# Kernel tuning notes

Hardware: AMD Instinct MI355X
Metric: run time of the kernel (lower is better)

## Reference

```python
import jax, jax.numpy as jnp
import numpy as np

N = 50000          # nodes
E = 800000         # edges (before self loops)
H = 4              # attention heads
C = 64             # per-head channels
D_IN = 256
NEG_ATT = 0.2      # GATConv attention LeakyReLU slope
NEG_ACT = 0.01     # nn.LeakyReLU default slope
EPS = 1e-5
MLP_DIMS = [64, 32, 16, 2]


def _gat_layer(x, src, dst, W, a_src, a_dst, b, concat):
    """PyG GATConv: gather -> segment-softmax over dst -> scatter-add."""
    n = x.shape[0]
    h = (x @ W).reshape(n, H, C)                       # [N,H,C]
    s = (h * a_src).sum(-1)                            # [N,H]
    d = (h * a_dst).sum(-1)                            # [N,H]
    e = jax.nn.leaky_relu(s[src] + d[dst], NEG_ATT)    # [E',H]
    m = jax.ops.segment_max(e, dst, num_segments=n)    # per-dst max (self loops -> no empty segs)
    w = jnp.exp(e - m[dst])
    den = jax.ops.segment_sum(w, dst, num_segments=n)
    alpha = w / den[dst]                               # [E',H]
    out = jax.ops.segment_sum(alpha[:, :, None] * h[src], dst, num_segments=n)  # [N,H,C]
    out = out.reshape(n, H * C) if concat else out.mean(axis=1)
    return out + b


def _graph_norm(x, w, b, a):
    mu = x.mean(axis=0, keepdims=True)
    y = x - a * mu
    var = (y * y).mean(axis=0, keepdims=True)
    return w * y * jax.lax.rsqrt(var + EPS) + b


def setup_inputs() -> dict:
    key = jax.random.key(0)
    ks = jax.random.split(key, 40)
    d = {
        'x': jax.random.normal(ks[0], (N, D_IN), dtype=jnp.float32),
        'edge_index': jax.random.randint(ks[1], (2, E), 0, N, dtype=jnp.int64),
    }
    dims_in = [D_IN, H * C, H * C]
    norm_dims = [H * C, H * C, C]
    k = 2
    for i in range(3):
        fan = dims_in[i]
        d[f'W{i}'] = jax.random.normal(ks[k], (fan, H * C), dtype=jnp.float32) / np.sqrt(fan); k += 1
        d[f'as{i}'] = jax.random.normal(ks[k], (H, C), dtype=jnp.float32) / np.sqrt(C); k += 1
        d[f'ad{i}'] = jax.random.normal(ks[k], (H, C), dtype=jnp.float32) / np.sqrt(C); k += 1
        d[f'b{i}'] = jnp.zeros((norm_dims[i],), dtype=jnp.float32)
        d[f'gw{i}'] = jnp.ones((norm_dims[i],), dtype=jnp.float32)
        d[f'gb{i}'] = jnp.zeros((norm_dims[i],), dtype=jnp.float32)
        d[f'ga{i}'] = jnp.ones((norm_dims[i],), dtype=jnp.float32)
    for j in range(3):
        fi, fo = MLP_DIMS[j], MLP_DIMS[j + 1]
        d[f'mW{j}'] = jax.random.normal(ks[k], (fi, fo), dtype=jnp.float32) / np.sqrt(fi); k += 1
        d[f'mb{j}'] = jnp.zeros((fo,), dtype=jnp.float32)
    return d


def reference(x, edge_index,
              W0, as0, ad0, b0, gw0, gb0, ga0,
              W1, as1, ad1, b1, gw1, gb1, ga1,
              W2, as2, ad2, b2, gw2, gb2, ga2,
              mW0, mb0, mW1, mb1, mW2, mb2):
    n = x.shape[0]
    loop = jnp.arange(n, dtype=edge_index.dtype)
    src = jnp.concatenate([edge_index[0], loop])   # add self loops (PyG default)
    dst = jnp.concatenate([edge_index[1], loop])

    h = _gat_layer(x, src, dst, W0, as0, ad0, b0, concat=True)
    h = jax.nn.leaky_relu(_graph_norm(h, gw0, gb0, ga0), NEG_ACT)
    h = _gat_layer(h, src, dst, W1, as1, ad1, b1, concat=True)
    h = jax.nn.leaky_relu(_graph_norm(h, gw1, gb1, ga1), NEG_ACT)
    h = _gat_layer(h, src, dst, W2, as2, ad2, b2, concat=False)
    h = jax.nn.leaky_relu(_graph_norm(h, gw2, gb2, ga2), NEG_ACT)

    h = jax.nn.relu(h @ mW0 + mb0)
    h = jax.nn.relu(h @ mW1 + mb1)
    return h @ mW2 + mb2
```

## Files before the change

### kernel.cpp

```cpp
#include <hip/hip_runtime.h>

#define NN 50000
#define EE 800000
#define ET 850000
#define HH 4
#define CC 64
#define FDIM 256

#define SCAN_BLK 512
#define SCAN_NB ((NN + SCAN_BLK - 1) / SCAN_BLK)

typedef unsigned short ushort;
typedef __bf16 bf16x8 __attribute__((ext_vector_type(8)));
typedef float floatx4 __attribute__((ext_vector_type(4)));
typedef ushort ushort8v __attribute__((ext_vector_type(8)));
struct ushort4s { ushort x, y, z, w; };

__device__ __forceinline__ ushort f2bf(float f) {
  union { float f; unsigned u; } v; v.f = f;
  unsigned r = v.u + 0x7fffu + ((v.u >> 16) & 1u);
  return (ushort)(r >> 16);
}
__device__ __forceinline__ float bf2f(ushort u) {
  return __uint_as_float(((unsigned)u) << 16);
}

__device__ __forceinline__ int get_edge(const void* p, int is64, long long idx) {
  if (is64) return (int)((const long long*)p)[idx];
  return ((const int*)p)[idx];
}

__global__ void detect_kernel(const unsigned int* p, int* flag) {
  __shared__ unsigned red[256];
  int t = threadIdx.x;
  unsigned o = 0;
  for (int i = 0; i < 4; i++) o |= p[(t * 4 + i) * 2 + 1];
  red[t] = o;
  __syncthreads();
  for (int s = 128; s > 0; s >>= 1) {
    if (t < s) red[t] |= red[t + s];
    __syncthreads();
  }
  if (t == 0) *flag = (red[0] == 0) ? 1 : 0;
}

__global__ void degree_kernel(const void* eidx, const int* flag, int* deg) {
  int k = blockIdx.x * blockDim.x + threadIdx.x;
  if (k >= ET) return;
  int is64 = *flag;
  int dst = (k < EE) ? get_edge(eidx, is64, (long long)EE + k) : (k - EE);
  atomicAdd(&deg[dst], 1);
}

__global__ __launch_bounds__(SCAN_BLK) void scan1_kernel(const int* __restrict__ deg,
                                                         int* __restrict__ rowptr,
                                                         int* __restrict__ bsum) {
  __shared__ int sm[SCAN_BLK];
  int t = threadIdx.x;
  int i = blockIdx.x * SCAN_BLK + t;
  int v = (i < NN) ? deg[i] : 0;
  sm[t] = v;
  __syncthreads();
#pragma unroll
  for (int o = 1; o < SCAN_BLK; o <<= 1) {
    int u = (t >= o) ? sm[t - o] : 0;
    __syncthreads();
    sm[t] += u;
    __syncthreads();
  }
  if (i < NN) rowptr[i] = sm[t] - v;
  if (t == SCAN_BLK - 1) bsum[blockIdx.x] = sm[t];
}

__global__ __launch_bounds__(128) void scan2_kernel(const int* __restrict__ bsum,
                                                    int* __restrict__ boff,
                                                    int* __restrict__ rowptr) {
  __shared__ int sm[128];
  int t = threadIdx.x;
  int v = (t < SCAN_NB) ? bsum[t] : 0;
  sm[t] = v;
  __syncthreads();
#pragma unroll
  for (int o = 1; o < 128; o <<= 1) {
    int u = (t >= o) ? sm[t - o] : 0;
    __syncthreads();
    sm[t] += u;
    __syncthreads();
  }
  if (t < SCAN_NB) boff[t] = sm[t] - v;
  if (t == 0) rowptr[NN] = ET;
}

__global__ __launch_bounds__(SCAN_BLK) void scan3_kernel(int* __restrict__ rowptr,
                                                         int* __restrict__ cursor,
                                                         const int* __restrict__ boff) {
  int i = blockIdx.x * SCAN_BLK + threadIdx.x;
  if (i >= NN) return;
  int v = rowptr[i] + boff[blockIdx.x];
  rowptr[i] = v;
  cursor[i] = v;
}

__global__ void fill_kernel(const void* eidx, const int* flag, int* cursor, int* csr_src) {
  int k = blockIdx.x * blockDim.x + threadIdx.x;
  if (k >= ET) return;
  int is64 = *flag;
  int src, dst;
  if (k < EE) {
    src = get_edge(eidx, is64, k);
    dst = get_edge(eidx, is64, (long long)EE + k);
  } else {
    src = dst = k - EE;
  }
  int pos = atomicAdd(&cursor[dst], 1);
  csr_src[pos] = src;
}

__global__ void conv_w_kernel(const float* __restrict__ W0, const float* __restrict__ W1,
                              const float* __restrict__ W2,
                              ushort* __restrict__ T0, ushort* __restrict__ T1,
                              ushort* __restrict__ T2) {
  const float* W = (blockIdx.y == 0) ? W0 : (blockIdx.y == 1) ? W1 : W2;
  ushort* Wt = (blockIdx.y == 0) ? T0 : (blockIdx.y == 1) ? T1 : T2;
  int idx = blockIdx.x * 256 + threadIdx.x;
  int k = idx >> 8, n = idx & 255;
  Wt[n * 256 + k] = f2bf(W[idx]);
}

template <int MODE>
__global__ __launch_bounds__(256) void gemm_bf16(const void* __restrict__ Ap,
                                                 const ushort* __restrict__ Bt,
                                                 ushort* __restrict__ C,
                                                 const float* __restrict__ as_,
                                                 const float* __restrict__ ad_,
                                                 float* __restrict__ s_arr,
                                                 float* __restrict__ d_arr,
                                                 const float* __restrict__ colsum,
                                                 const float* __restrict__ colsumsq,
                                                 const float* __restrict__ ga,
                                                 const float* __restrict__ gw,
                                                 const float* __restrict__ gb) {
  __shared__ ushort As[4 * 512];
  __shared__ ushort Bs[8 * 512];
  __shared__ float scs[FDIM], shs[FDIM];
  int tid = threadIdx.x, w = tid >> 6, l = tid & 63;
  int brow0 = blockIdx.x * 64, bcol0 = blockIdx.y * 128;
  int lm = l & 15, lk = (l >> 4) * 8;
  int arA = min(brow0 + w * 16 + lm, NN - 1);
  size_t arowA = (size_t)arA * 256 + lk;
  const ushort* bg0 = Bt + (size_t)(bcol0 + (2 * w) * 16 + lm) * 256 + lk;
  const ushort* bg1 = Bt + (size_t)(bcol0 + (2 * w + 1) * 16 + lm) * 256 + lk;

  if constexpr (MODE == 1) {
    const float invn = 1.0f / (float)NN;
    float mu = colsum[tid] * invn;
    float ex2 = colsumsq[tid] * invn;
    float a = ga[tid];
    float var = fmaxf(ex2 - (2.f * a - a * a) * mu * mu, 0.f);
    float s = gw[tid] * rsqrtf(var + 1e-5f);
    scs[tid] = s;
    shs[tid] = gb[tid] - s * a * mu;
    __syncthreads();
  }

  floatx4 acc[2][4];
#pragma unroll
  for (int i = 0; i < 2; i++)
#pragma unroll
    for (int j = 0; j < 4; j++) acc[i][j] = floatx4{0.f, 0.f, 0.f, 0.f};

  int wm = (w >> 1) * 2, wn = (w & 1) * 4;

  for (int k0 = 0; k0 < 256; k0 += 32) {
    ushort8v a0;
    if constexpr (MODE == 0) {
      const float* p0 = (const float*)Ap + arowA + k0;
      float4 u0 = *(const float4*)p0, v0 = *(const float4*)(p0 + 4);
      a0 = ushort8v{f2bf(u0.x), f2bf(u0.y), f2bf(u0.z), f2bf(u0.w),
                    f2bf(v0.x), f2bf(v0.y), f2bf(v0.z), f2bf(v0.w)};
    } else {
      ushort8v r0 = *(const ushort8v*)((const ushort*)Ap + arowA + k0);
      int kb = k0 + lk;
#pragma unroll
      for (int j = 0; j < 8; j++) {
        float sc = scs[kb + j], sh = shs[kb + j];
        float y0 = fmaf(sc, bf2f(r0[j]), sh);
        y0 = fmaxf(y0, 0.01f * y0);
        a0[j] = f2bf(y0);
      }
    }
    ushort8v b0 = *(const ushort8v*)(bg0 + k0);
    ushort8v b1 = *(const ushort8v*)(bg1 + k0);
    *(ushort8v*)&As[w * 512 + l * 8] = a0;
    *(ushort8v*)&Bs[(2 * w) * 512 + l * 8] = b0;
    *(ushort8v*)&Bs[(2 * w + 1) * 512 + l * 8] = b1;
    __syncthreads();
    bf16x8 af[2], bfr[4];
#pragma unroll
    for (int i = 0; i < 2; i++) af[i] = *(const bf16x8*)&As[(wm + i) * 512 + l * 8];
#pragma unroll
    for (int j = 0; j < 4; j++) bfr[j] = *(const bf16x8*)&Bs[(wn + j) * 512 + l * 8];
#pragma unroll
    for (int i = 0; i < 2; i++)
#pragma unroll
      for (int j = 0; j < 4; j++)
        acc[i][j] = __builtin_amdgcn_mfma_f32_16x16x32_bf16(af[i], bfr[j], acc[i][j], 0, 0, 0);
    __syncthreads();
  }

  int quad = l >> 4;
#pragma unroll
  for (int i = 0; i < 2; i++) {
    int r0 = brow0 + (wm + i) * 16 + quad * 4;
#pragma unroll
    for (int j = 0; j < 4; j++) {
      int col = bcol0 + (wn + j) * 16 + lm;
#pragma unroll
      for (int r = 0; r < 4; r++) {
        int row = r0 + r;
        if (row < NN) C[(size_t)row * 256 + col] = f2bf(acc[i][j][r]);
      }
    }
  }
  float asv[4], adv[4];
#pragma unroll
  for (int j = 0; j < 4; j++) {
    int col = bcol0 + (wn + j) * 16 + lm;
    asv[j] = as_[col];
    adv[j] = ad_[col];
  }
  int head = (bcol0 >> 6) + (w & 1);
#pragma unroll
  for (int i = 0; i < 2; i++) {
#pragma unroll
    for (int r = 0; r < 4; r++) {
      float sp = acc[i][0][r] * asv[0] + acc[i][1][r] * asv[1] +
                 acc[i][2][r] * asv[2] + acc[i][3][r] * asv[3];
      float dp = acc[i][0][r] * adv[0] + acc[i][1][r] * adv[1] +
                 acc[i][2][r] * adv[2] + acc[i][3][r] * adv[3];
      sp += __shfl_xor(sp, 1); dp += __shfl_xor(dp, 1);
      sp += __shfl_xor(sp, 2); dp += __shfl_xor(dp, 2);
      sp += __shfl_xor(sp, 4); dp += __shfl_xor(dp, 4);
      sp += __shfl_xor(sp, 8); dp += __shfl_xor(dp, 8);
      if (lm == 0) {
        int row = brow0 + (wm + i) * 16 + quad * 4 + r;
        if (row < NN) {
          s_arr[row * HH + head] = sp;
          d_arr[row * HH + head] = dp;
        }
      }
    }
  }
}

template <bool CONCAT>
__global__ __launch_bounds__(256) void agg_kernel(const ushort* __restrict__ hb,
                                                  const float* __restrict__ s_arr,
                                                  const float* __restrict__ d_arr,
                                                  const int* __restrict__ rowptr,
                                                  const int* __restrict__ csr_src,
                                                  const float* __restrict__ bias,
                                                  void* __restrict__ outp) {
  int w = __builtin_amdgcn_readfirstlane(threadIdx.x >> 6);
  int l = threadIdx.x & 63;
  int head = l >> 4;
  int n = blockIdx.x * 4 + w;
  int beg = rowptr[n], end = rowptr[n + 1];
  float dh = d_arr[n * HH + head];
  float a0 = 0.f, a1 = 0.f, a2 = 0.f, a3 = 0.f, den = 0.f;

  int i = beg;
  for (; i + 8 <= end; i += 8) {
    int s0 = csr_src[i], s1 = csr_src[i + 1], s2 = csr_src[i + 2], s3 = csr_src[i + 3];
    int s4 = csr_src[i + 4], s5 = csr_src[i + 5], s6 = csr_src[i + 6], s7 = csr_src[i + 7];
    float e0 = s_arr[s0 * HH + head] + dh;
    float e1 = s_arr[s1 * HH + head] + dh;
    float e2 = s_arr[s2 * HH + head] + dh;
    float e3 = s_arr[s3 * HH + head] + dh;
    float e4 = s_arr[s4 * HH + head] + dh;
    float e5 = s_arr[s5 * HH + head] + dh;
    float e6 = s_arr[s6 * HH + head] + dh;
    float e7 = s_arr[s7 * HH + head] + dh;
    ushort4s h0 = *(const ushort4s*)(hb + (unsigned)(s0 * FDIM + l * 4));
    ushort4s h1 = *(const ushort4s*)(hb + (unsigned)(s1 * FDIM + l * 4));
    ushort4s h2 = *(const ushort4s*)(hb + (unsigned)(s2 * FDIM + l * 4));
    ushort4s h3 = *(const ushort4s*)(hb + (unsigned)(s3 * FDIM + l * 4));
    ushort4s h4 = *(const ushort4s*)(hb + (unsigned)(s4 * FDIM + l * 4));
    ushort4s h5 = *(const ushort4s*)(hb + (unsigned)(s5 * FDIM + l * 4));
    ushort4s h6 = *(const ushort4s*)(hb + (unsigned)(s6 * FDIM + l * 4));
    ushort4s h7 = *(const ushort4s*)(hb + (unsigned)(s7 * FDIM + l * 4));
    e0 = (e0 > 0.f) ? e0 : 0.2f * e0;  float w0 = __expf(e0);
    e1 = (e1 > 0.f) ? e1 : 0.2f * e1;  float w1 = __expf(e1);
    e2 = (e2 > 0.f) ? e2 : 0.2f * e2;  float w2 = __expf(e2);
    e3 = (e3 > 0.f) ? e3 : 0.2f * e3;  float w3 = __expf(e3);
    e4 = (e4 > 0.f) ? e4 : 0.2f * e4;  float w4 = __expf(e4);
    e5 = (e5 > 0.f) ? e5 : 0.2f * e5;  float w5 = __expf(e5);
    e6 = (e6 > 0.f) ? e6 : 0.2f * e6;  float w6 = __expf(e6);
    e7 = (e7 > 0.f) ? e7 : 0.2f * e7;  float w7 = __expf(e7);
    den += ((w0 + w1) + (w2 + w3)) + ((w4 + w5) + (w6 + w7));
    a0 = fmaf(w0, bf2f(h0.x), a0); a1 = fmaf(w0, bf2f(h0.y), a1);
    a2 = fmaf(w0, bf2f(h0.z), a2); a3 = fmaf(w0, bf2f(h0.w), a3);
    a0 = fmaf(w1, bf2f(h1.x), a0); a1 = fmaf(w1, bf2f(h1.y), a1);
    a2 = fmaf(w1, bf2f(h1.z), a2); a3 = fmaf(w1, bf2f(h1.w), a3);
    a0 = fmaf(w2, bf2f(h2.x), a0); a1 = fmaf(w2, bf2f(h2.y), a1);
    a2 = fmaf(w2, bf2f(h2.z), a2); a3 = fmaf(w2, bf2f(h2.w), a3);
    a0 = fmaf(w3, bf2f(h3.x), a0); a1 = fmaf(w3, bf2f(h3.y), a1);
    a2 = fmaf(w3, bf2f(h3.z), a2); a3 = fmaf(w3, bf2f(h3.w), a3);
    a0 = fmaf(w4, bf2f(h4.x), a0); a1 = fmaf(w4, bf2f(h4.y), a1);
    a2 = fmaf(w4, bf2f(h4.z), a2); a3 = fmaf(w4, bf2f(h4.w), a3);
    a0 = fmaf(w5, bf2f(h5.x), a0); a1 = fmaf(w5, bf2f(h5.y), a1);
    a2 = fmaf(w5, bf2f(h5.z), a2); a3 = fmaf(w5, bf2f(h5.w), a3);
    a0 = fmaf(w6, bf2f(h6.x), a0); a1 = fmaf(w6, bf2f(h6.y), a1);
    a2 = fmaf(w6, bf2f(h6.z), a2); a3 = fmaf(w6, bf2f(h6.w), a3);
    a0 = fmaf(w7, bf2f(h7.x), a0); a1 = fmaf(w7, bf2f(h7.y), a1);
    a2 = fmaf(w7, bf2f(h7.z), a2); a3 = fmaf(w7, bf2f(h7.w), a3);
  }
  for (; i + 4 <= end; i += 4) {
    int s0 = csr_src[i], s1 = csr_src[i + 1], s2 = csr_src[i + 2], s3 = csr_src[i + 3];
    float e0 = s_arr[s0 * HH + head] + dh;
    float e1 = s_arr[s1 * HH + head] + dh;
    float e2 = s_arr[s2 * HH + head] + dh;
    float e3 = s_arr[s3 * HH + head] + dh;
    ushort4s h0 = *(const ushort4s*)(hb + (unsigned)(s0 * FDIM + l * 4));
    ushort4s h1 = *(const ushort4s*)(hb + (unsigned)(s1 * FDIM + l * 4));
    ushort4s h2 = *(const ushort4s*)(hb + (unsigned)(s2 * FDIM + l * 4));
    ushort4s h3 = *(const ushort4s*)(hb + (unsigned)(s3 * FDIM + l * 4));
    e0 = (e0 > 0.f) ? e0 : 0.2f * e0;  float w0 = __expf(e0);
    e1 = (e1 > 0.f) ? e1 : 0.2f * e1;  float w1 = __expf(e1);
    e2 = (e2 > 0.f) ? e2 : 0.2f * e2;  float w2 = __expf(e2);
    e3 = (e3 > 0.f) ? e3 : 0.2f * e3;  float w3 = __expf(e3);
    den += (w0 + w1) + (w2 + w3);
    a0 = fmaf(w0, bf2f(h0.x), a0); a1 = fmaf(w0, bf2f(h0.y), a1);
    a2 = fmaf(w0, bf2f(h0.z), a2); a3 = fmaf(w0, bf2f(h0.w), a3);
    a0 = fmaf(w1, bf2f(h1.x), a0); a1 = fmaf(w1, bf2f(h1.y), a1);
    a2 = fmaf(w1, bf2f(h1.z), a2); a3 = fmaf(w1, bf2f(h1.w), a3);
    a0 = fmaf(w2, bf2f(h2.x), a0); a1 = fmaf(w2, bf2f(h2.y), a1);
    a2 = fmaf(w2, bf2f(h2.z), a2); a3 = fmaf(w2, bf2f(h2.w), a3);
    a0 = fmaf(w3, bf2f(h3.x), a0); a1 = fmaf(w3, bf2f(h3.y), a1);
    a2 = fmaf(w3, bf2f(h3.z), a2); a3 = fmaf(w3, bf2f(h3.w), a3);
  }
  for (; i < end; i++) {
    int s0 = csr_src[i];
    float e0 = s_arr[s0 * HH + head] + dh;
    ushort4s h0 = *(const ushort4s*)(hb + (unsigned)(s0 * FDIM + l * 4));
    e0 = (e0 > 0.f) ? e0 : 0.2f * e0;
    float w0 = __expf(e0);
    den += w0;
    a0 = fmaf(w0, bf2f(h0.x), a0); a1 = fmaf(w0, bf2f(h0.y), a1);
    a2 = fmaf(w0, bf2f(h0.z), a2); a3 = fmaf(w0, bf2f(h0.w), a3);
  }
  float inv = 1.0f / den;
  float r0 = a0 * inv, r1 = a1 * inv, r2 = a2 * inv, r3 = a3 * inv;

  if (CONCAT) {
    float4 bv = ((const float4*)bias)[l];
    ushort4s o;
    o.x = f2bf(r0 + bv.x); o.y = f2bf(r1 + bv.y);
    o.z = f2bf(r2 + bv.z); o.w = f2bf(r3 + bv.w);
    ((ushort4s*)outp)[(unsigned)(n * 64 + l)] = o;
  } else {
    r0 += __shfl_xor(r0, 16); r1 += __shfl_xor(r1, 16);
    r2 += __shfl_xor(r2, 16); r3 += __shfl_xor(r3, 16);
    r0 += __shfl_xor(r0, 32); r1 += __shfl_xor(r1, 32);
    r2 += __shfl_xor(r2, 32); r3 += __shfl_xor(r3, 32);
    if (l < 16) {
      float4 bv = ((const float4*)bias)[l];
      float4 o;
      o.x = 0.25f * r0 + bv.x; o.y = 0.25f * r1 + bv.y;
      o.z = 0.25f * r2 + bv.z; o.w = 0.25f * r3 + bv.w;
      ((float4*)outp)[(unsigned)(n * 16 + l)] = o;
    }
  }
}

__global__ __launch_bounds__(256) void norm_reduce_bf(const ushort* __restrict__ xin,
                                                      float* colsum, float* colsumsq) {
  __shared__ float4 sm1[256], sm2[256];
  int t = threadIdx.x;
  int c4 = (t & 63) * 4;
  int rl = t >> 6;
  int r0 = blockIdx.x * 128;
  int r1 = min(NN, r0 + 128);
  float s0 = 0.f, s1 = 0.f, s2 = 0.f, s3 = 0.f;
  float q0 = 0.f, q1 = 0.f, q2 = 0.f, q3 = 0.f;
  for (int r = r0 + rl; r < r1; r += 4) {
    ushort4s v = *(const ushort4s*)(xin + (size_t)r * FDIM + c4);
    float f0 = bf2f(v.x), f1 = bf2f(v.y), f2 = bf2f(v.z), f3 = bf2f(v.w);
    s0 += f0; q0 += f0 * f0;
    s1 += f1; q1 += f1 * f1;
    s2 += f2; q2 += f2 * f2;
    s3 += f3; q3 += f3 * f3;
  }
  sm1[t] = float4{s0, s1, s2, s3};
  sm2[t] = float4{q0, q1, q2, q3};
  __syncthreads();
  if (t < 64) {
    float4 a = sm1[t], b = sm1[t + 64], c = sm1[t + 128], d = sm1[t + 192];
    atomicAdd(&colsum[c4 + 0], a.x + b.x + c.x + d.x);
    atomicAdd(&colsum[c4 + 1], a.y + b.y + c.y + d.y);
    atomicAdd(&colsum[c4 + 2], a.z + b.z + c.z + d.z);
    atomicAdd(&colsum[c4 + 3], a.w + b.w + c.w + d.w);
    float4 e = sm2[t], f = sm2[t + 64], g = sm2[t + 128], h = sm2[t + 192];
    atomicAdd(&colsumsq[c4 + 0], e.x + f.x + g.x + h.x);
    atomicAdd(&colsumsq[c4 + 1], e.y + f.y + g.y + h.y);
    atomicAdd(&colsumsq[c4 + 2], e.z + f.z + g.z + h.z);
    atomicAdd(&colsumsq[c4 + 3], e.w + f.w + g.w + h.w);
  }
}

__global__ __launch_bounds__(256) void norm_reduce_f32(const float* __restrict__ xin,
                                                       float* colsum, float* colsumsq) {
  int f = threadIdx.x & (CC - 1);
  int rl = threadIdx.x / CC;
  int r0 = blockIdx.x * 128;
  int r1 = min(NN, r0 + 128);
  float s1 = 0.f, s2 = 0.f;
  for (int r = r0 + rl; r < r1; r += 4) {
    float v = xin[(size_t)r * CC + f];
    s1 += v; s2 += v * v;
  }
  atomicAdd(&colsum[f], s1);
  atomicAdd(&colsumsq[f], s2);
}

__global__ __launch_bounds__(256) void mlp_kernel(const float* __restrict__ xin,
                                                  const float* __restrict__ colsum,
                                                  const float* __restrict__ colsumsq,
                                                  const float* __restrict__ ga,
                                                  const float* __restrict__ gw,
                                                  const float* __restrict__ gb,
                                                  const float* mW0, const float* mb0,
                                                  const float* mW1, const float* mb1,
                                                  const float* mW2, const float* mb2,
                                                  float* __restrict__ out) {
  __shared__ float W0s[64 * 32];
  __shared__ float W1s[32 * 16];
  __shared__ float W2s[16 * 2];
  __shared__ float b0s[32], b1s[16], b2s[2];
  __shared__ float sc[CC], sh[CC];
  int t = threadIdx.x;
  for (int i = t; i < 2048; i += 256) W0s[i] = mW0[i];
  for (int i = t; i < 512; i += 256) W1s[i] = mW1[i];
  if (t < 32) { W2s[t] = mW2[t]; b0s[t] = mb0[t]; }
  if (t < 16) b1s[t] = mb1[t];
  if (t < 2) b2s[t] = mb2[t];
  if (t < CC) {
    const float invn = 1.0f / (float)NN;
    float mu = colsum[t] * invn;
    float ex2 = colsumsq[t] * invn;
    float a = ga[t];
    float var = fmaxf(ex2 - (2.f * a - a * a) * mu * mu, 0.f);
    float s = gw[t] * rsqrtf(var + 1e-5f);
    sc[t] = s; sh[t] = gb[t] - s * a * mu;
  }
  __syncthreads();
  int node = blockIdx.x * 256 + t;
  if (node >= NN) return;
  float in[64];
  const float* xr = xin + (size_t)node * 64;
#pragma unroll
  for (int k = 0; k < 64; k++) {
    float y = sc[k] * xr[k] + sh[k];
    in[k] = (y > 0.f) ? y : 0.01f * y;
  }
  float h1[32];
#pragma unroll
  for (int j = 0; j < 32; j++) h1[j] = b0s[j];
#pragma unroll
  for (int k = 0; k < 64; k++) {
    float v = in[k];
#pragma unroll
    for (int j = 0; j < 32; j++) h1[j] += v * W0s[k * 32 + j];
  }
#pragma unroll
  for (int j = 0; j < 32; j++) h1[j] = fmaxf(h1[j], 0.f);
  float h2[16];
#pragma unroll
  for (int j = 0; j < 16; j++) h2[j] = b1s[j];
#pragma unroll
  for (int k = 0; k < 32; k++) {
    float v = h1[k];
#pragma unroll
    for (int j = 0; j < 16; j++) h2[j] += v * W1s[k * 16 + j];
  }
#pragma unroll
  for (int j = 0; j < 16; j++) h2[j] = fmaxf(h2[j], 0.f);
  float o0 = b2s[0], o1 = b2s[1];
#pragma unroll
  for (int k = 0; k < 16; k++) {
    o0 += h2[k] * W2s[k * 2 + 0];
    o1 += h2[k] * W2s[k * 2 + 1];
  }
  out[(size_t)node * 2 + 0] = o0;
  out[(size_t)node * 2 + 1] = o1;
}

extern "C" void kernel_launch(void* const* d_in, const int* in_sizes, int n_in,
                              void* d_out, int out_size, void* d_ws, size_t ws_size,
                              hipStream_t stream) {
  const float* x = (const float*)d_in[0];
  const void* ei = d_in[1];
  const float* W[3]   = {(const float*)d_in[2],  (const float*)d_in[9],  (const float*)d_in[16]};
  const float* as_[3] = {(const float*)d_in[3],  (const float*)d_in[10], (const float*)d_in[17]};
  const float* ad_[3] = {(const float*)d_in[4],  (const float*)d_in[11], (const float*)d_in[18]};
  const float* b_[3]  = {(const float*)d_in[5],  (const float*)d_in[12], (const float*)d_in[19]};
  const float* gw[3]  = {(const float*)d_in[6],  (const float*)d_in[13], (const float*)d_in[20]};
  const float* gb[3]  = {(const float*)d_in[7],  (const float*)d_in[14], (const float*)d_in[21]};
  const float* ga[3]  = {(const float*)d_in[8],  (const float*)d_in[15], (const float*)d_in[22]};
  const float* mW0 = (const float*)d_in[23];
  const float* mb0 = (const float*)d_in[24];
  const float* mW1 = (const float*)d_in[25];
  const float* mb1 = (const float*)d_in[26];
  const float* mW2 = (const float*)d_in[27];
  const float* mb2 = (const float*)d_in[28];
  float* out = (float*)d_out;

  char* ws = (char*)d_ws;
  size_t off = 0;
  auto take = [&](size_t bytes) -> char* {
    char* p = ws + off;
    off = (off + bytes + 255) & ~(size_t)255;
    return p;
  };
  ushort* hb    = (ushort*)take((size_t)NN * FDIM * 2);
  ushort* aggb  = (ushort*)take((size_t)NN * FDIM * 2);
  float* bufD   = (float*)take((size_t)NN * CC * 4);
  ushort* Wt[3];
  for (int i = 0; i < 3; i++) Wt[i] = (ushort*)take((size_t)256 * 256 * 2);
  float* s_arr  = (float*)take((size_t)NN * HH * 4);
  float* d_arr  = (float*)take((size_t)NN * HH * 4);
  char* zbase   = (char*)take(0);
  int* deg      = (int*)take((size_t)NN * 4);
  float* cs[3];
  for (int i = 0; i < 3; i++) cs[i] = (float*)take(2048);
  size_t zlen   = (size_t)(((char*)cs[2] + 2048) - zbase);
  int* cursor   = (int*)take((size_t)NN * 4);
  int* rowptr   = (int*)take((size_t)(NN + 1) * 4);
  int* csr_src  = (int*)take((size_t)ET * 4);
  int* bsum     = (int*)take(512);
  int* boff     = (int*)take(512);
  int* flag     = (int*)take(256);

  hipMemsetAsync(zbase, 0, zlen, stream);

  detect_kernel<<<1, 256, 0, stream>>>((const unsigned int*)ei, flag);
  degree_kernel<<<(ET + 255) / 256, 256, 0, stream>>>(ei, flag, deg);
  scan1_kernel<<<SCAN_NB, SCAN_BLK, 0, stream>>>(deg, rowptr, bsum);
  scan2_kernel<<<1, 128, 0, stream>>>(bsum, boff, rowptr);
  scan3_kernel<<<SCAN_NB, SCAN_BLK, 0, stream>>>(rowptr, cursor, boff);
  fill_kernel<<<(ET + 255) / 256, 256, 0, stream>>>(ei, flag, cursor, csr_src);

  conv_w_kernel<<<dim3(256, 3), 256, 0, stream>>>(W[0], W[1], W[2], Wt[0], Wt[1], Wt[2]);

  dim3 ggrid((NN + 63) / 64, 2);
  for (int L = 0; L < 3; L++) {
    if (L == 0)
      gemm_bf16<0><<<ggrid, 256, 0, stream>>>((const void*)x, Wt[0], hb,
                                              as_[0], ad_[0], s_arr, d_arr,
                                              nullptr, nullptr, nullptr, nullptr, nullptr);
    else
      gemm_bf16<1><<<ggrid, 256, 0, stream>>>((const void*)aggb, Wt[L], hb,
                                              as_[L], ad_[L], s_arr, d_arr,
                                              cs[L - 1], cs[L - 1] + 256,
                                              ga[L - 1], gw[L - 1], gb[L - 1]);
    if (L < 2) {
      agg_kernel<true><<<NN / 4, 256, 0, stream>>>(hb, s_arr, d_arr, rowptr, csr_src, b_[L], aggb);
      norm_reduce_bf<<<(NN + 127) / 128, 256, 0, stream>>>(aggb, cs[L], cs[L] + 256);
    } else {
      agg_kernel<false><<<NN / 4, 256, 0, stream>>>(hb, s_arr, d_arr, rowptr, csr_src, b_[L], bufD);
      norm_reduce_f32<<<(NN + 127) / 128, 256, 0, stream>>>(bufD, cs[2], cs[2] + 256);
    }
  }
  mlp_kernel<<<(NN + 255) / 256, 256, 0, stream>>>(bufD, cs[2], cs[2] + 256,
                                                   ga[2], gw[2], gb[2],
                                                   mW0, mb0, mW1, mb1, mW2, mb2, out);
}
```

Before: 690.8 us.

## Split wavefront into two half-waves aggregating disjoint edges with 16-byte loads

The aggregation kernel now splits each 64-lane wavefront into two 32-lane halves, each handling a different group of four edges. Each lane loads 8 bf16 values (16 bytes) per neighbor instead of 4. Partial sums and denominators are combined across halves with a cross-lane shuffle. This widens the gather loads and doubles edge-level parallelism per wave, at the cost of extra shuffles, more accumulator registers, and a masked tail that issues redundant loads.

Result: no change. 697.0 us (+0.9%).

```diff
diff --git a/kernel.cpp b/kernel.cpp
--- a/kernel.cpp
+++ b/kernel.cpp
@@ -263,112 +263,94 @@
                                                   void* __restrict__ outp) {
   int w = __builtin_amdgcn_readfirstlane(threadIdx.x >> 6);
   int l = threadIdx.x & 63;
-  int head = l >> 4;
+  int half = l >> 5;
+  int ll = l & 31;
+  int head = ll >> 3;
   int n = blockIdx.x * 4 + w;
   int beg = rowptr[n], end = rowptr[n + 1];
   float dh = d_arr[n * HH + head];
-  float a0 = 0.f, a1 = 0.f, a2 = 0.f, a3 = 0.f, den = 0.f;
-
-  int i = beg;
-  for (; i + 8 <= end; i += 8) {
-    int s0 = csr_src[i], s1 = csr_src[i + 1], s2 = csr_src[i + 2], s3 = csr_src[i + 3];
-    int s4 = csr_src[i + 4], s5 = csr_src[i + 5], s6 = csr_src[i + 6], s7 = csr_src[i + 7];
+  float a[8];
+#pragma unroll
+  for (int j = 0; j < 8; j++) a[j] = 0.f;
+  float den = 0.f;
+
+  int cnt = end - beg;
+  int main_end = beg + (cnt & ~7);
+
+  for (int b0 = beg; b0 < main_end; b0 += 8) {
+    int i0 = b0 + half * 4;
+    int s0 = csr_src[i0], s1 = csr_src[i0 + 1], s2 = csr_src[i0 + 2], s3 = csr_src[i0 + 3];
     float e0 = s_arr[s0 * HH + head] + dh;
     float e1 = s_arr[s1 * HH + head] + dh;
     float e2 = s_arr[s2 * HH + head] + dh;
     float e3 = s_arr[s3 * HH + head] + dh;
-    float e4 = s_arr[s4 * HH + head] + dh;
-    float e5 = s_arr[s5 * HH + head] + dh;
-    float e6 = s_arr[s6 * HH + head] + dh;
-    float e7 = s_arr[s7 * HH + head] + dh;
-    ushort4s h0 = *(const ushort4s*)(hb + (unsigned)(s0 * FDIM + l * 4));
-    ushort4s h1 = *(const ushort4s*)(hb + (unsigned)(s1 * FDIM + l * 4));
-    ushort4s h2 = *(const ushort4s*)(hb + (unsigned)(s2 * FDIM + l * 4));
-    ushort4s h3 = *(const ushort4s*)(hb + (unsigned)(s3 * FDIM + l * 4));
-    ushort4s h4 = *(const ushort4s*)(hb + (unsigned)(s4 * FDIM + l * 4));
-    ushort4s h5 = *(const ushort4s*)(hb + (unsigned)(s5 * FDIM + l * 4));
-    ushort4s h6 = *(const ushort4s*)(hb + (unsigned)(s6 * FDIM + l * 4));
-    ushort4s h7 = *(const ushort4s*)(hb + (unsigned)(s7 * FDIM + l * 4));
-    e0 = (e0 > 0.f) ? e0 : 0.2f * e0;  float w0 = __expf(e0);
-    e1 = (e1 > 0.f) ? e1 : 0.2f * e1;  float w1 = __expf(e1);
-    e2 = (e2 > 0.f) ? e2 : 0.2f * e2;  float w2 = __expf(e2);
-    e3 = (e3 > 0.f) ? e3 : 0.2f * e3;  float w3 = __expf(e3);
-    e4 = (e4 > 0.f) ? e4 : 0.2f * e4;  float w4 = __expf(e4);
-    e5 = (e5 > 0.f) ? e5 : 0.2f * e5;  float w5 = __expf(e5);
-    e6 = (e6 > 0.f) ? e6 : 0.2f * e6;  float w6 = __expf(e6);
-    e7 = (e7 > 0.f) ? e7 : 0.2f * e7;  float w7 = __expf(e7);
-    den += ((w0 + w1) + (w2 + w3)) + ((w4 + w5) + (w6 + w7));
-    a0 = fmaf(w0, bf2f(h0.x), a0); a1 = fmaf(w0, bf2f(h0.y), a1);
-    a2 = fmaf(w0, bf2f(h0.z), a2); a3 = fmaf(w0, bf2f(h0.w), a3);
-    a0 = fmaf(w1, bf2f(h1.x), a0); a1 = fmaf(w1, bf2f(h1.y), a1);
-    a2 = fmaf(w1, bf2f(h1.z), a2); a3 = fmaf(w1, bf2f(h1.w), a3);
-    a0 = fmaf(w2, bf2f(h2.x), a0); a1 = fmaf(w2, bf2f(h2.y), a1);
-    a2 = fmaf(w2, bf2f(h2.z), a2); a3 = fmaf(w2, bf2f(h2.w), a3);
-    a0 = fmaf(w3, bf2f(h3.x), a0); a1 = fmaf(w3, bf2f(h3.y), a1);
-    a2 = fmaf(w3, bf2f(h3.z), a2); a3 = fmaf(w3, bf2f(h3.w), a3);
-    a0 = fmaf(w4, bf2f(h4.x), a0); a1 = fmaf(w4, bf2f(h4.y), a1);
-    a2 = fmaf(w4, bf2f(h4.z), a2); a3 = fmaf(w4, bf2f(h4.w), a3);
-    a0 = fmaf(w5, bf2f(h5.x), a0); a1 = fmaf(w5, bf2f(h5.y), a1);
-    a2 = fmaf(w5, bf2f(h5.z), a2); a3 = fmaf(w5, bf2f(h5.w), a3);
-    a0 = fmaf(w6, bf2f(h6.x), a0); a1 = fmaf(w6, bf2f(h6.y), a1);
-    a2 = fmaf(w6, bf2f(h6.z), a2); a3 = fmaf(w6, bf2f(h6.w), a3);
-    a0 = fmaf(w7, bf2f(h7.x), a0); a1 = fmaf(w7, bf2f(h7.y), a1);
-    a2 = fmaf(w7, bf2f(h7.z), a2); a3 = fmaf(w7, bf2f(h7.w), a3);
-  }
-  for (; i + 4 <= end; i += 4) {
-    int s0 = csr_src[i], s1 = csr_src[i + 1], s2 = csr_src[i + 2], s3 = csr_src[i + 3];
-    float e0 = s_arr[s0 * HH + head] + dh;
-    float e1 = s_arr[s1 * HH + head] + dh;
-    float e2 = s_arr[s2 * HH + head] + dh;
-    float e3 = s_arr[s3 * HH + head] + dh;
-    ushort4s h0 = *(const ushort4s*)(hb + (unsigned)(s0 * FDIM + l * 4));
-    ushort4s h1 = *(const ushort4s*)(hb + (unsigned)(s1 * FDIM + l * 4));
-    ushort4s h2 = *(const ushort4s*)(hb + (unsigned)(s2 * FDIM + l * 4));
-    ushort4s h3 = *(const ushort4s*)(hb + (unsigned)(s3 * FDIM + l * 4));
+    ushort8v h0 = *(const ushort8v*)(hb + (unsigned)(s0 * FDIM) + ll * 8);
+    ushort8v h1 = *(const ushort8v*)(hb + (unsigned)(s1 * FDIM) + ll * 8);
+    ushort8v h2 = *(const ushort8v*)(hb + (unsigned)(s2 * FDIM) + ll * 8);
+    ushort8v h3 = *(const ushort8v*)(hb + (unsigned)(s3 * FDIM) + ll * 8);
     e0 = (e0 > 0.f) ? e0 : 0.2f * e0;  float w0 = __expf(e0);
     e1 = (e1 > 0.f) ? e1 : 0.2f * e1;  float w1 = __expf(e1);
     e2 = (e2 > 0.f) ? e2 : 0.2f * e2;  float w2 = __expf(e2);
     e3 = (e3 > 0.f) ? e3 : 0.2f * e3;  float w3 = __expf(e3);
     den += (w0 + w1) + (w2 + w3);
-    a0 = fmaf(w0, bf2f(h0.x), a0); a1 = fmaf(w0, bf2f(h0.y), a1);
-    a2 = fmaf(w0, bf2f(h0.z), a2); a3 = fmaf(w0, bf2f(h0.w), a3);
-    a0 = fmaf(w1, bf2f(h1.x), a0); a1 = fmaf(w1, bf2f(h1.y), a1);
-    a2 = fmaf(w1, bf2f(h1.z), a2); a3 = fmaf(w1, bf2f(h1.w), a3);
-    a0 = fmaf(w2, bf2f(h2.x), a0); a1 = fmaf(w2, bf2f(h2.y), a1);
-    a2 = fmaf(w2, bf2f(h2.z), a2); a3 = fmaf(w2, bf2f(h2.w), a3);
-    a0 = fmaf(w3, bf2f(h3.x), a0); a1 = fmaf(w3, bf2f(h3.y), a1);
-    a2 = fmaf(w3, bf2f(h3.z), a2); a3 = fmaf(w3, bf2f(h3.w), a3);
-  }
-  for (; i < end; i++) {
-    int s0 = csr_src[i];
-    float e0 = s_arr[s0 * HH + head] + dh;
-    ushort4s h0 = *(const ushort4s*)(hb + (unsigned)(s0 * FDIM + l * 4));
-    e0 = (e0 > 0.f) ? e0 : 0.2f * e0;
-    float w0 = __expf(e0);
-    den += w0;
-    a0 = fmaf(w0, bf2f(h0.x), a0); a1 = fmaf(w0, bf2f(h0.y), a1);
-    a2 = fmaf(w0, bf2f(h0.z), a2); a3 = fmaf(w0, bf2f(h0.w), a3);
-  }
+#pragma unroll
+    for (int j = 0; j < 8; j++) {
+      a[j] = fmaf(w0, bf2f(h0[j]), a[j]);
+      a[j] = fmaf(w1, bf2f(h1[j]), a[j]);
+      a[j] = fmaf(w2, bf2f(h2[j]), a[j]);
+      a[j] = fmaf(w3, bf2f(h3[j]), a[j]);
+    }
+  }
+  if (main_end < end) {
+    int i0 = main_end + half * 4;
+#pragma unroll
+    for (int t = 0; t < 4; t++) {
+      int idx = i0 + t;
+      int sid = csr_src[(idx < end) ? idx : (end - 1)];
+      float e0 = s_arr[sid * HH + head] + dh;
+      ushort8v h0 = *(const ushort8v*)(hb + (unsigned)(sid * FDIM) + ll * 8);
+      e0 = (e0 > 0.f) ? e0 : 0.2f * e0;
+      float w0 = (idx < end) ? __expf(e0) : 0.f;
+      den += w0;
+#pragma unroll
+      for (int j = 0; j < 8; j++) a[j] = fmaf(w0, bf2f(h0[j]), a[j]);
+    }
+  }
+
+  den += __shfl_xor(den, 32);
   float inv = 1.0f / den;
-  float r0 = a0 * inv, r1 = a1 * inv, r2 = a2 * inv, r3 = a3 * inv;
+#pragma unroll
+  for (int j = 0; j < 8; j++) {
+    a[j] += __shfl_xor(a[j], 32);
+    a[j] *= inv;
+  }
 
   if (CONCAT) {
-    float4 bv = ((const float4*)bias)[l];
-    ushort4s o;
-    o.x = f2bf(r0 + bv.x); o.y = f2bf(r1 + bv.y);
-    o.z = f2bf(r2 + bv.z); o.w = f2bf(r3 + bv.w);
-    ((ushort4s*)outp)[(unsigned)(n * 64 + l)] = o;
+    if (half == 0) {
+      float4 bv0 = ((const float4*)bias)[ll * 2];
+      float4 bv1 = ((const float4*)bias)[ll * 2 + 1];
+      ushort8v o;
+      o[0] = f2bf(a[0] + bv0.x); o[1] = f2bf(a[1] + bv0.y);
+      o[2] = f2bf(a[2] + bv0.z); o[3] = f2bf(a[3] + bv0.w);
+      o[4] = f2bf(a[4] + bv1.x); o[5] = f2bf(a[5] + bv1.y);
+      o[6] = f2bf(a[6] + bv1.z); o[7] = f2bf(a[7] + bv1.w);
+      *(ushort8v*)((ushort*)outp + (size_t)n * FDIM + ll * 8) = o;
+    }
   } else {
-    r0 += __shfl_xor(r0, 16); r1 += __shfl_xor(r1, 16);
-    r2 += __shfl_xor(r2, 16); r3 += __shfl_xor(r3, 16);
-    r0 += __shfl_xor(r0, 32); r1 += __shfl_xor(r1, 32);
-    r2 += __shfl_xor(r2, 32); r3 += __shfl_xor(r3, 32);
-    if (l < 16) {
-      float4 bv = ((const float4*)bias)[l];
-      float4 o;
-      o.x = 0.25f * r0 + bv.x; o.y = 0.25f * r1 + bv.y;
-      o.z = 0.25f * r2 + bv.z; o.w = 0.25f * r3 + bv.w;
-      ((float4*)outp)[(unsigned)(n * 16 + l)] = o;
+#pragma unroll
+    for (int j = 0; j < 8; j++) {
+      a[j] += __shfl_xor(a[j], 8);
+      a[j] += __shfl_xor(a[j], 16);
+    }
+    if (l < 8) {
+      const float4* bp = (const float4*)bias;
+      float4 b0 = bp[l * 2], b1 = bp[l * 2 + 1];
+      float4 o0{0.25f * a[0] + b0.x, 0.25f * a[1] + b0.y,
+                0.25f * a[2] + b0.z, 0.25f * a[3] + b0.w};
+      float4 o1{0.25f * a[4] + b1.x, 0.25f * a[5] + b1.y,
+                0.25f * a[6] + b1.z, 0.25f * a[7] + b1.w};
+      ((float4*)outp)[(size_t)n * 16 + l * 2] = o0;
+      ((float4*)outp)[(size_t)n * 16 + l * 2 + 1] = o1;
     }
   }
 }
```
